# Kernel optimization log

Hardware: AMD Instinct MI355X
Metric: run time of the kernel (lower is better)

Reference implementation:

```python
import jax, jax.numpy as jnp
import numpy as np

SEQ_LEN = 4096
NUM_EIGH = 40
D_IN = 64
D_OUT = 64
K_U = 3
BSZ = 2


def _spectral_filters(L, K):
    # Hankel matrix Z_ij = 2/((i+j)^3 - (i+j)), i,j in [1, L]
    e = np.arange(1, L + 1, dtype=np.float64)
    s = e[:, None] + e[None, :]
    Z = 2.0 / (s ** 3 - s)
    sigma, phi = np.linalg.eigh(Z)
    phi_k = phi[:, -K:] * sigma[-K:] ** 0.25  # (L, K)
    return jnp.asarray(phi_k, dtype=jnp.float32)


def setup_inputs() -> dict:
    key = jax.random.key(0)
    kx, km, kp, kn = jax.random.split(key, 4)
    x = jax.random.normal(kx, (BSZ, SEQ_LEN, D_IN), dtype=jnp.float32)
    phi = _spectral_filters(SEQ_LEN, NUM_EIGH)  # (L, K)
    M = jax.random.normal(km, (D_OUT, D_IN, K_U), dtype=jnp.float32) / D_IN
    M_phi_plus = jax.random.normal(kp, (NUM_EIGH, D_IN, D_OUT), dtype=jnp.float32) / 10.0
    M_phi_minus = jax.random.normal(kn, (NUM_EIGH, D_IN, D_OUT), dtype=jnp.float32) / 10.0
    return {"x": x, "phi": phi, "M": M, "M_phi_plus": M_phi_plus, "M_phi_minus": M_phi_minus}


def _stu_forward(x, phi, M, M_phi_plus, M_phi_minus):
    bsz, L, d_in = x.shape
    n = int(2 ** np.ceil(np.log2(2 * L - 1)))  # FFT length (8192)
    t = jnp.arange(L)
    sgn = jnp.where(t % 2 == 1, -1.0, 1.0).astype(x.dtype)  # (L,)

    # FFT of [u, u*sgn] once over d_in (K-expansion deferred to freq domain; FFT is linear)
    U = jnp.stack([x, x * sgn[None, :, None]], axis=-1)        # (b, L, d, 2)
    U_f = jnp.fft.rfft(U, n=n, axis=1)                         # (b, nf, d, 2)
    v_f = jnp.fft.rfft(phi.astype(jnp.float32), n=n, axis=0)   # (nf, K)

    prod = v_f[None, :, :, None, None] * U_f[:, :, None, :, :]  # (b, nf, K, d, 2)
    U_conv = jnp.fft.irfft(prod, n=n, axis=1)[:, :L]            # (b, L, K, d, 2)
    U_plus = U_conv[..., 0]
    U_minus = U_conv[..., 1] * sgn[None, :, None, None]

    # spectral tensordot: contract (K, d_in) -> d_out
    spec = (jnp.einsum('blkd,kdo->blo', U_plus, M_phi_plus)
            + jnp.einsum('blkd,kdo->blo', U_minus, M_phi_minus))

    ar = jnp.zeros((bsz, L, M.shape[0]), dtype=x.dtype)
    for i in range(M.shape[2]):  # k_u is small and fixed
        y_i = jnp.einsum('bli,oi->blo', x, M[:, :, i])
        if i > 0:
            y_i = jnp.pad(y_i[:, : L - i], ((0, 0), (i, 0), (0, 0)))
        ar = ar + y_i
    return spec + ar


def reference(x, phi, M, M_phi_plus, M_phi_minus):
    return _stu_forward(x, phi, M, M_phi_plus, M_phi_minus)
```

## Files before the change

### kernel.cpp

```cpp
#include <hip/hip_runtime.h>

typedef short bf16x8 __attribute__((ext_vector_type(8)));
typedef float f32x4 __attribute__((ext_vector_type(4)));
typedef unsigned short u16;

__device__ __forceinline__ u16 f2bf(float f) {
    unsigned u = __builtin_bit_cast(unsigned, f);
    return (u16)((u + 0x7fffu + ((u >> 16) & 1u)) >> 16);
}

__global__ __launch_bounds__(256)
void k_pre(const float* __restrict__ Mp, const float* __restrict__ Mm,
           float* __restrict__ ApT, float* __restrict__ AmT,
           float* __restrict__ out, int* __restrict__ counter) {
    __shared__ float tp[64 * 65], tm[64 * 65];
    if (blockIdx.x < 40) {
        const int k = blockIdx.x, tid = threadIdx.x;
        for (int f = tid; f < 4096; f += 256) {
            int d = f >> 6, o = f & 63;
            float p = Mp[k * 4096 + f], m = Mm[k * 4096 + f];
            tp[o * 65 + d] = p + m;
            tm[o * 65 + d] = p - m;
        }
        __syncthreads();
        for (int f = tid; f < 4096; f += 256) {
            int o = f >> 6, d = f & 63;
            ApT[k * 4096 + f] = tp[o * 65 + d];
            AmT[k * 4096 + f] = tm[o * 65 + d];
        }
    } else {
        const int bz = blockIdx.x - 40;
        if (bz == 0 && threadIdx.x == 0) *counter = 0;
        float* po = out + bz * 4096;
        #pragma unroll
        for (int i = 0; i < 4; ++i)
            *(f32x4*)(po + (threadIdx.x + i * 256) * 4) = (f32x4){0.f, 0.f, 0.f, 0.f};
    }
}

__global__ __launch_bounds__(256)
void k_mid(const float* __restrict__ x, u16* __restrict__ xpad,
           const float* __restrict__ phi, const float* __restrict__ ApT,
           const float* __restrict__ AmT, const float* __restrict__ Mar,
           u16* __restrict__ wg) {
    if (blockIdx.x < 256) {
        const int u = blockIdx.x;
        #pragma unroll
        for (int i = 0; i < 4; ++i) {
            int gid = (u * 4 + i) * 256 + threadIdx.x;
            int b = gid >> 17, rem = gid & 131071;
            int r = rem >> 4, c4 = rem & 15;
            u16 o0 = 0, o1 = 0, o2 = 0, o3 = 0;
            if (r >= 4096) {
                const f32x4 v = *(const f32x4*)(x + ((b << 12) + (r - 4096)) * 64 + c4 * 4);
                o0 = f2bf(v.x); o1 = f2bf(v.y); o2 = f2bf(v.z); o3 = f2bf(v.w);
            }
            u16* p = xpad + ((b << 13) + r) * 64 + c4 * 4;
            p[0] = o0; p[1] = o1; p[2] = o2; p[3] = o3;
        }
    } else {
        const int bi  = blockIdx.x - 256;
        const int par = bi & 1;
        const int sbq = bi >> 1;
        const int sb  = sbq >> 4, qb = sbq & 15;
        const int q   = qb * 256 + threadIdx.x;
        const int o   = q >> 6, d = q & 63;
        const float* A = (par ? AmT : ApT);

        float a[40];
        #pragma unroll
        for (int k = 0; k < 40; ++k) a[k] = A[k * 4096 + q];

        #pragma unroll 2
        for (int m = 0; m < 32; ++m) {
            const int s = sb * 64 + 2 * m + par;
            const float* ph = phi + s * 40;
            float e0 = 0.f, e1 = 0.f;
            #pragma unroll
            for (int k = 0; k < 40; k += 2) { e0 += ph[k] * a[k]; e1 += ph[k + 1] * a[k + 1]; }
            float ev = e0 + e1;
            if (s < 3) ev += Mar[o * 192 + d * 3 + s];
            wg[(size_t)s * 4096 + q] = f2bf(ev);
        }
    }
}

__global__ __launch_bounds__(256, 2)
void k_spectral(const u16* __restrict__ xpad, const u16* __restrict__ wg,
                float* __restrict__ out, int* __restrict__ counter) {
    __shared__ __align__(16) u16 xs[2 * 191 * 64];
    __shared__ __align__(16) u16 wsm[2 * 64 * 64];
    __shared__ int sh;

    const int tid  = threadIdx.x;
    const int lane = tid & 63, w = tid >> 6;
    const int m15  = lane & 15, q4 = lane >> 4;
    const int par  = w >> 1, batch = w & 1;
    const int f0 = tid * 2, f1 = tid * 2 + 1;
    const int l0 = (((f0 >> 3) * 8) + ((f0 & 7) ^ ((f0 >> 3) & 7))) * 8;
    const int l1 = (((f1 >> 3) * 8) + ((f1 & 7) ^ ((f1 >> 3) & 7))) * 8;

    for (;;) {
        __syncthreads();
        if (tid == 0) sh = atomicAdd(counter, 1);
        __syncthreads();
        const int U = sh;
        if (U >= 1120) break;

        int mu = U, shalf = 0, slen = 64;
        if (U >= 992) { mu = 992 + ((U - 992) >> 1); shalf = (U - 992) & 1; slen = 32; }
        int g = 0;
        #pragma unroll 1
        while (g < 31 && (g + 1) * (64 - g) <= mu) ++g;
        const int rem = mu - g * (65 - g);
        const int cnt = 32 - g;
        const int col = (rem >= cnt) ? 1 : 0;
        const int J = 2 * g + col;
        const int I = g + (col ? rem - cnt : rem);
        const int t0 = I << 7, s0 = (J << 6) + (shalf << 5);
        const int nrows = 127 + slen;
        const int jmax = slen >> 1;
        const int base = 4096 + t0 - s0 - (slen - 1);

        const u16* wbase = wg + (size_t)s0 * 4096;
        bf16x8 pre[4];
        pre[0] = *(const bf16x8*)(wbase + f0 * 8);
        pre[1] = *(const bf16x8*)(wbase + f1 * 8);
        pre[2] = *(const bf16x8*)(wbase + 4096 + f0 * 8);
        pre[3] = *(const bf16x8*)(wbase + 4096 + f1 * 8);

        #pragma unroll
        for (int b = 0; b < 2; ++b) {
            #pragma unroll 1
            for (int f = tid; f < nrows * 8; f += 256) {
                int r = f >> 3, c = f & 7;
                bf16x8 v = *(const bf16x8*)(xpad + (size_t)((b << 13) + base + r) * 64 + c * 8);
                *(bf16x8*)(xs + ((b * 191 + r) * 8 + (c ^ (r & 7))) * 8) = v;
            }
        }

        f32x4 acc[8][4];
        #pragma unroll
        for (int mt = 0; mt < 8; ++mt)
            #pragma unroll
            for (int nt = 0; nt < 4; ++nt)
                acc[mt][nt] = (f32x4){0.f, 0.f, 0.f, 0.f};

        const u16* xb = xs + batch * (191 * 64);

        #pragma unroll 1
        for (int j = 0; j < jmax; ++j) {
            __syncthreads();
            *(bf16x8*)(wsm + l0)        = pre[0];
            *(bf16x8*)(wsm + l1)        = pre[1];
            *(bf16x8*)(wsm + 4096 + l0) = pre[2];
            *(bf16x8*)(wsm + 4096 + l1) = pre[3];
            __syncthreads();
            if (j < jmax - 1) {
                const u16* wp = wbase + (size_t)(2 * j + 2) * 4096;
                pre[0] = *(const bf16x8*)(wp + f0 * 8);
                pre[1] = *(const bf16x8*)(wp + f1 * 8);
                pre[2] = *(const bf16x8*)(wp + 4096 + f0 * 8);
                pre[3] = *(const bf16x8*)(wp + 4096 + f1 * 8);
            }
            const u16* wpar = wsm + par * 4096;
            const int ds = 2 * j + par;
            #pragma unroll
            for (int ks = 0; ks < 2; ++ks) {
                const int kq = ks * 4 + q4;
                bf16x8 bf[4];
                #pragma unroll
                for (int nt = 0; nt < 4; ++nt) {
                    int o = nt * 16 + m15;
                    bf[nt] = *(const bf16x8*)(wpar + (o * 8 + (kq ^ (o & 7))) * 8);
                }
                #pragma unroll
                for (int mt = 0; mt < 8; ++mt) {
                    int r = mt * 16 + m15 + (slen - 1) - ds;
                    bf16x8 av = *(const bf16x8*)(xb + (r * 8 + (kq ^ (r & 7))) * 8);
                    #pragma unroll
                    for (int nt = 0; nt < 4; ++nt)
                        acc[mt][nt] = __builtin_amdgcn_mfma_f32_16x16x32_bf16(
                            av, bf[nt], acc[mt][nt], 0, 0, 0);
                }
            }
        }

        float* fs = (float*)wsm;
        #pragma unroll
        for (int rd = 0; rd < 4; ++rd) {
            __syncthreads();
            if (par == 1) {
                #pragma unroll
                for (int i = 0; i < 8; ++i) {
                    int ti = rd * 8 + i;
                    *(f32x4*)(fs + (batch * 8 + i) * 256 + lane * 4) = acc[ti >> 2][ti & 3];
                }
            }
            __syncthreads();
            if (par == 0) {
                #pragma unroll
                for (int i = 0; i < 8; ++i) {
                    int ti = rd * 8 + i;
                    f32x4 v = *(const f32x4*)(fs + (batch * 8 + i) * 256 + lane * 4);
                    acc[ti >> 2][ti & 3] += v;
                }
            }
        }

        if (par == 0) {
            #pragma unroll
            for (int mt = 0; mt < 8; ++mt) {
                int t = t0 + mt * 16 + q4 * 4;
                #pragma unroll
                for (int nt = 0; nt < 4; ++nt) {
                    int o = nt * 16 + m15;
                    float* op = out + (size_t)((batch << 12) + t) * 64 + o;
                    #pragma unroll
                    for (int r = 0; r < 4; ++r)
                        atomicAdd(op + r * 64, acc[mt][nt][r]);
                }
            }
        }
    }
}

extern "C" void kernel_launch(void* const* d_in, const int* in_sizes, int n_in,
                              void* d_out, int out_size, void* d_ws, size_t ws_size,
                              hipStream_t stream) {
    const float* x   = (const float*)d_in[0];
    const float* phi = (const float*)d_in[1];
    const float* M   = (const float*)d_in[2];
    const float* Mp  = (const float*)d_in[3];
    const float* Mm  = (const float*)d_in[4];
    float* out = (float*)d_out;

    int* counter = (int*)d_ws;
    u16* xpad = (u16*)((char*)d_ws + 4096);
    u16* wg   = (u16*)((char*)d_ws + 4096 + 2097152);
    float* ApT = (float*)((char*)d_ws + 4096 + 2097152 + 33554432);
    float* AmT = ApT + 40 * 4096;

    k_pre<<<168, 256, 0, stream>>>(Mp, Mm, ApT, AmT, out, counter);
    k_mid<<<2304, 256, 0, stream>>>(x, xpad, phi, ApT, AmT, M, wg);
    k_spectral<<<512, 256, 0, stream>>>(xpad, wg, out, counter);
}
```

Before: 220.6 us.

## Pre-swizzle spectral weights into MFMA fragment layout and load them directly to registers

The weight-generation kernel now writes the bf16 Toeplitz weights in a layout matching the MFMA B-operand fragments, so each lane in k_spectral loads its fragments straight from global memory into registers. The shared-memory weight staging, its per-step barriers, and the cross-wave reduction through LDS are removed. Work is now split so each wave pair handles a 64-row half of the time tile over all shifts, rather than splitting shifts by parity and summing afterwards. Weight loads are double-buffered in registers. The trade-off is that every wave fetches the full weight tile from global/L2 memory (four times per block) and the kernel needs more vector registers.

```diff
diff --git a/kernel.cpp b/kernel.cpp
--- a/kernel.cpp
+++ b/kernel.cpp
@@ -67,6 +67,10 @@
         const int o   = q >> 6, d = q & 63;
         const float* A = (par ? AmT : ApT);
 
+        const int nt_  = o >> 4, m15_ = o & 15;
+        const int ks_  = d >> 5, q4_ = (d >> 3) & 3, e_ = d & 7;
+        const int pidx = ((ks_ * 4 + nt_) * 64 + (q4_ * 16 + m15_)) * 8 + e_;
+
         float a[40];
         #pragma unroll
         for (int k = 0; k < 40; ++k) a[k] = A[k * 4096 + q];
@@ -80,7 +84,7 @@
             for (int k = 0; k < 40; k += 2) { e0 += ph[k] * a[k]; e1 += ph[k + 1] * a[k + 1]; }
             float ev = e0 + e1;
             if (s < 3) ev += Mar[o * 192 + d * 3 + s];
-            wg[(size_t)s * 4096 + q] = f2bf(ev);
+            wg[(size_t)s * 4096 + pidx] = f2bf(ev);
         }
     }
 }
@@ -89,16 +93,12 @@
 void k_spectral(const u16* __restrict__ xpad, const u16* __restrict__ wg,
                 float* __restrict__ out, int* __restrict__ counter) {
     __shared__ __align__(16) u16 xs[2 * 191 * 64];
-    __shared__ __align__(16) u16 wsm[2 * 64 * 64];
     __shared__ int sh;
 
     const int tid  = threadIdx.x;
     const int lane = tid & 63, w = tid >> 6;
     const int m15  = lane & 15, q4 = lane >> 4;
-    const int par  = w >> 1, batch = w & 1;
-    const int f0 = tid * 2, f1 = tid * 2 + 1;
-    const int l0 = (((f0 >> 3) * 8) + ((f0 & 7) ^ ((f0 >> 3) & 7))) * 8;
-    const int l1 = (((f1 >> 3) * 8) + ((f1 & 7) ^ ((f1 >> 3) & 7))) * 8;
+    const int th   = w >> 1, batch = w & 1;
 
     for (;;) {
         __syncthreads();
@@ -119,15 +119,7 @@
         const int I = g + (col ? rem - cnt : rem);
         const int t0 = I << 7, s0 = (J << 6) + (shalf << 5);
         const int nrows = 127 + slen;
-        const int jmax = slen >> 1;
         const int base = 4096 + t0 - s0 - (slen - 1);
-
-        const u16* wbase = wg + (size_t)s0 * 4096;
-        bf16x8 pre[4];
-        pre[0] = *(const bf16x8*)(wbase + f0 * 8);
-        pre[1] = *(const bf16x8*)(wbase + f1 * 8);
-        pre[2] = *(const bf16x8*)(wbase + 4096 + f0 * 8);
-        pre[3] = *(const bf16x8*)(wbase + 4096 + f1 * 8);
 
         #pragma unroll
         for (int b = 0; b < 2; ++b) {
@@ -138,88 +130,66 @@
                 *(bf16x8*)(xs + ((b * 191 + r) * 8 + (c ^ (r & 7))) * 8) = v;
             }
         }
-
-        f32x4 acc[8][4];
-        #pragma unroll
-        for (int mt = 0; mt < 8; ++mt)
+        __syncthreads();
+
+        f32x4 acc[4][4];
+        #pragma unroll
+        for (int mt = 0; mt < 4; ++mt)
             #pragma unroll
             for (int nt = 0; nt < 4; ++nt)
                 acc[mt][nt] = (f32x4){0.f, 0.f, 0.f, 0.f};
 
         const u16* xb = xs + batch * (191 * 64);
-
+        const int rb = th * 64 + (slen - 1) + m15;
+
+#define LOADW(BUF, S)                                                          \
+        {                                                                      \
+            const u16* wp_ = wg + (size_t)(S) * 4096 + lane * 8;               \
+            _Pragma("unroll")                                                  \
+            for (int f = 0; f < 8; ++f) BUF[f] = *(const bf16x8*)(wp_ + f * 512); \
+        }
+
+#define COMPUTE_S(BUF, DS)                                                     \
+        {                                                                      \
+            const int ds_ = (DS);                                              \
+            _Pragma("unroll")                                                  \
+            for (int ks = 0; ks < 2; ++ks) {                                   \
+                const int kq = ks * 4 + q4;                                    \
+                _Pragma("unroll")                                              \
+                for (int mt = 0; mt < 4; ++mt) {                               \
+                    int r = rb + mt * 16 - ds_;                                \
+                    bf16x8 av = *(const bf16x8*)(xb + (r * 8 + (kq ^ (r & 7))) * 8); \
+                    acc[mt][0] = __builtin_amdgcn_mfma_f32_16x16x32_bf16(av, BUF[ks * 4 + 0], acc[mt][0], 0, 0, 0); \
+                    acc[mt][1] = __builtin_amdgcn_mfma_f32_16x16x32_bf16(av, BUF[ks * 4 + 1], acc[mt][1], 0, 0, 0); \
+                    acc[mt][2] = __builtin_amdgcn_mfma_f32_16x16x32_bf16(av, BUF[ks * 4 + 2], acc[mt][2], 0, 0, 0); \
+                    acc[mt][3] = __builtin_amdgcn_mfma_f32_16x16x32_bf16(av, BUF[ks * 4 + 3], acc[mt][3], 0, 0, 0); \
+                }                                                              \
+            }                                                                  \
+        }
+
+        bf16x8 b0[8], b1[8];
+        LOADW(b0, s0);
+        const int half = slen >> 1;
         #pragma unroll 1
-        for (int j = 0; j < jmax; ++j) {
-            __syncthreads();
-            *(bf16x8*)(wsm + l0)        = pre[0];
-            *(bf16x8*)(wsm + l1)        = pre[1];
-            *(bf16x8*)(wsm + 4096 + l0) = pre[2];
-            *(bf16x8*)(wsm + 4096 + l1) = pre[3];
-            __syncthreads();
-            if (j < jmax - 1) {
-                const u16* wp = wbase + (size_t)(2 * j + 2) * 4096;
-                pre[0] = *(const bf16x8*)(wp + f0 * 8);
-                pre[1] = *(const bf16x8*)(wp + f1 * 8);
-                pre[2] = *(const bf16x8*)(wp + 4096 + f0 * 8);
-                pre[3] = *(const bf16x8*)(wp + 4096 + f1 * 8);
-            }
-            const u16* wpar = wsm + par * 4096;
-            const int ds = 2 * j + par;
+        for (int jj = 0; jj < half; ++jj) {
+            LOADW(b1, s0 + 2 * jj + 1);
+            COMPUTE_S(b0, 2 * jj);
+            if (jj + 1 < half) LOADW(b0, s0 + 2 * jj + 2);
+            COMPUTE_S(b1, 2 * jj + 1);
+        }
+#undef LOADW
+#undef COMPUTE_S
+
+        #pragma unroll
+        for (int mt = 0; mt < 4; ++mt) {
+            int t = t0 + th * 64 + mt * 16 + q4 * 4;
             #pragma unroll
-            for (int ks = 0; ks < 2; ++ks) {
-                const int kq = ks * 4 + q4;
-                bf16x8 bf[4];
+            for (int nt = 0; nt < 4; ++nt) {
+                int o = nt * 16 + m15;
+                float* op = out + (size_t)((batch << 12) + t) * 64 + o;
                 #pragma unroll
-                for (int nt = 0; nt < 4; ++nt) {
-                    int o = nt * 16 + m15;
-                    bf[nt] = *(const bf16x8*)(wpar + (o * 8 + (kq ^ (o & 7))) * 8);
-                }
-                #pragma unroll
-                for (int mt = 0; mt < 8; ++mt) {
-                    int r = mt * 16 + m15 + (slen - 1) - ds;
-                    bf16x8 av = *(const bf16x8*)(xb + (r * 8 + (kq ^ (r & 7))) * 8);
-                    #pragma unroll
-                    for (int nt = 0; nt < 4; ++nt)
-                        acc[mt][nt] = __builtin_amdgcn_mfma_f32_16x16x32_bf16(
-                            av, bf[nt], acc[mt][nt], 0, 0, 0);
-                }
-            }
-        }
-
-        float* fs = (float*)wsm;
-        #pragma unroll
-        for (int rd = 0; rd < 4; ++rd) {
-            __syncthreads();
-            if (par == 1) {
-                #pragma unroll
-                for (int i = 0; i < 8; ++i) {
-                    int ti = rd * 8 + i;
-                    *(f32x4*)(fs + (batch * 8 + i) * 256 + lane * 4) = acc[ti >> 2][ti & 3];
-                }
-            }
-            __syncthreads();
-            if (par == 0) {
-                #pragma unroll
-                for (int i = 0; i < 8; ++i) {
-                    int ti = rd * 8 + i;
-                    f32x4 v = *(const f32x4*)(fs + (batch * 8 + i) * 256 + lane * 4);
-                    acc[ti >> 2][ti & 3] += v;
-                }
-            }
-        }
-
-        if (par == 0) {
-            #pragma unroll
-            for (int mt = 0; mt < 8; ++mt) {
-                int t = t0 + mt * 16 + q4 * 4;
-                #pragma unroll
-                for (int nt = 0; nt < 4; ++nt) {
-                    int o = nt * 16 + m15;
-                    float* op = out + (size_t)((batch << 12) + t) * 64 + o;
-                    #pragma unroll
-                    for (int r = 0; r < 4; ++r)
-                        atomicAdd(op + r * 64, acc[mt][nt][r]);
-                }
+                for (int r = 0; r < 4; ++r)
+                    atomicAdd(op + r * 64, acc[mt][nt][r]);
             }
         }
     }
```

Measured after the change: 225.7 us. +2.3%, slower.
